# Performance work log

Measured on AMD Instinct MI355X. Metric: run time of the kernel, lower is better.

Reference implementation:

```python
import jax, jax.numpy as jnp
import numpy as np

PS = 14            # patch size
EMBED = 1024       # vision embed dim
LLM = 2048         # llm embed dim
DS = 2             # downsample factor
B = 8
GRID = 64          # H = W = 64 patches per image
MAX_POS = 4096
ROPE_THETA = 10000.0


def _rope_cache(dim, max_pos, base):
    inv_freq = 1.0 / (base ** (jnp.arange(0, dim, 2, dtype=jnp.float32) / dim))
    t = jnp.arange(max_pos, dtype=jnp.float32)
    freqs = jnp.outer(t, inv_freq)  # [max_pos, dim//2]
    return jnp.cos(freqs), jnp.sin(freqs)


def setup_inputs() -> dict:
    key = jax.random.key(0)
    ks = jax.random.split(key, 5)
    n_total = B * GRID * GRID
    pixel_values = jax.random.normal(ks[0], (n_total, 3, PS, PS), jnp.float32)
    patch_w = jax.random.normal(ks[1], (EMBED, 3, PS, PS), jnp.float32) * (1.0 / np.sqrt(3 * PS * PS))
    patch_b = jax.random.normal(ks[2], (EMBED,), jnp.float32) * 0.02
    dense_w = jax.random.normal(ks[3], (LLM, EMBED, DS, DS), jnp.float32) * (1.0 / np.sqrt(EMBED * DS * DS))
    dense_b = jax.random.normal(ks[4], (LLM,), jnp.float32) * 0.02
    rope_dim = EMBED // 2
    cos_x, sin_x = _rope_cache(rope_dim, MAX_POS, ROPE_THETA)
    cos_y, sin_y = _rope_cache(rope_dim, MAX_POS, ROPE_THETA)
    grid_hw = jnp.full((B, 2), GRID, dtype=jnp.int32)
    return {"pixel_values": pixel_values, "grid_hw": grid_hw,
            "patch_w": patch_w, "patch_b": patch_b,
            "dense_w": dense_w, "dense_b": dense_b,
            "cos_x": cos_x, "sin_x": sin_x, "cos_y": cos_y, "sin_y": sin_y}


def _apply_rotary_1d(x, cos_c, sin_c, pos):
    # x: [N, d], cos_c/sin_c: [max_pos, d//2], pos: [N] int
    c = cos_c[pos]  # gather: [N, d//2]
    s = sin_c[pos]
    x1 = x[:, 0::2]
    x2 = x[:, 1::2]
    o1 = x1 * c - x2 * s
    o2 = x1 * s + x2 * c
    return jnp.stack([o1, o2], axis=-1).reshape(x.shape)  # re-interleave


def _positions(grid_np):
    # grid metadata is static host-side data; build per-patch (x, y) coords
    xs, ys = [], []
    for h, w in grid_np:
        pid = np.arange(h * w)
        xs.append(pid % w)
        ys.append(pid // w)
    return jnp.asarray(np.concatenate(xs)), jnp.asarray(np.concatenate(ys))


def reference(pixel_values, grid_hw, patch_w, patch_b, dense_w, dense_b,
              cos_x, sin_x, cos_y, sin_y):
    grid_np = np.asarray(grid_hw)
    # patchify conv (kernel == stride == patch) is a per-patch linear proj
    pe = jnp.einsum('nchw,echw->ne', pixel_values, patch_w) + patch_b  # [N, E]
    pe = jax.nn.gelu(pe, approximate=False)
    abs_x, abs_y = _positions(grid_np)
    half = EMBED // 2
    p1 = _apply_rotary_1d(pe[:, :half], cos_x, sin_x, abs_x)
    p2 = _apply_rotary_1d(pe[:, half:], cos_y, sin_y, abs_y)
    pe = jnp.concatenate([p1, p2], axis=-1)  # [N, E]
    # per-image downsample conv (kernel == stride == DS): 2x2 block linear
    outs = []
    cur = 0
    for h, w in grid_np:
        x = pe[cur:cur + h * w].reshape(h // DS, DS, w // DS, DS, EMBED)
        o = jnp.einsum('hpwqe,oepq->hwo', x, dense_w) + dense_b
        outs.append(o.reshape(-1, LLM))
        cur += h * w
    return jnp.concatenate(outs, axis=0)
```

## Files before the change

### kernel.cpp

```cpp
#include <hip/hip_runtime.h>
#include <cstdint>


using f16x8 = __attribute__((ext_vector_type(8))) _Float16;
using f32x4 = __attribute__((ext_vector_type(4))) float;

__device__ __forceinline__ void gload_lds16(const void* g, void* l) {
  __builtin_amdgcn_global_load_lds(
      reinterpret_cast<const __attribute__((address_space(1))) unsigned int*>(
          reinterpret_cast<uintptr_t>(g)),
      reinterpret_cast<__attribute__((address_space(3))) unsigned int*>(
          reinterpret_cast<uintptr_t>(l)),
      16, 0, 0);
}

#define BAR   asm volatile("s_barrier" ::: "memory")
#define LGKM0 asm volatile("s_waitcnt lgkmcnt(0)" ::: "memory")
#define VM0   asm volatile("s_waitcnt vmcnt(0)" ::: "memory")

#define KP 640


__global__ void conv_b1_kernel(const float* __restrict__ w1,
                               _Float16* __restrict__ h) {
  int i = blockIdx.x * 256 + threadIdx.x;
  if (i >= 1024 * KP) return;
  int e = i / KP;
  int k = i - e * KP;
  float v = (k < 588) ? w1[(size_t)e * 588 + k] : 0.0f;
  h[i] = (_Float16)v;
}

__global__ void conv_b2_kernel(const float* __restrict__ w2,
                               _Float16* __restrict__ h) {
  int i = blockIdx.x * 256 + threadIdx.x;
  int o   = i >> 12;
  int rem = i & 4095;
  int pq  = rem >> 10;
  int e   = rem & 1023;
  h[i] = (_Float16)w2[(size_t)o * 4096 + e * 4 + pq];
}

__global__ void conv_pix_kernel(const float* __restrict__ pix,
                                _Float16* __restrict__ h) {
  int i = blockIdx.x * 256 + threadIdx.x;
  if (i >= 32768 * (KP / 8)) return;
  int n = i / (KP / 8);
  int g = i - n * (KP / 8);
  int k0 = g * 8;
  f16x8 v;
  if (k0 + 8 <= 588) {
    const float4 x0 = *(const float4*)(pix + (size_t)n * 588 + k0);
    const float4 x1 = *(const float4*)(pix + (size_t)n * 588 + k0 + 4);
    v[0] = (_Float16)x0.x; v[1] = (_Float16)x0.y;
    v[2] = (_Float16)x0.z; v[3] = (_Float16)x0.w;
    v[4] = (_Float16)x1.x; v[5] = (_Float16)x1.y;
    v[6] = (_Float16)x1.z; v[7] = (_Float16)x1.w;
  } else {
#pragma unroll
    for (int j = 0; j < 8; ++j) {
      int k = k0 + j;
      v[j] = (k < 588) ? (_Float16)pix[(size_t)n * 588 + k] : (_Float16)0.0f;
    }
  }
  *(f16x8*)(h + (size_t)n * KP + k0) = v;
}


#define MFMA16(I0, J0, AV, BV)                                                \
  _Pragma("unroll") for (int i_ = 0; i_ < 4; ++i_)                            \
  _Pragma("unroll") for (int j_ = 0; j_ < 2; ++j_)                            \
  _Pragma("unroll") for (int k_ = 0; k_ < 2; ++k_)                            \
      acc[(I0) + i_][(J0) + j_] = __builtin_amdgcn_mfma_f32_16x16x32_f16(     \
          AV[i_][k_], BV[j_][k_], acc[(I0) + i_][(J0) + j_], 0, 0, 0);

#define TILE_BODY(sb)                                                         \
  {                                                                           \
    f16x8 a0[4][2], a1[4][2], vb0[2][2], vb1[2][2];                           \
    _Pragma("unroll") for (int i = 0; i < 4; ++i) {                           \
      a0[i][0] = *(const f16x8*)(lbase + (sb) + aoff + i * 2048 + so0);       \
      a0[i][1] = *(const f16x8*)(lbase + (sb) + aoff + i * 2048 + so1);       \
    }                                                                         \
    _Pragma("unroll") for (int j = 0; j < 2; ++j) {                           \
      vb0[j][0] = *(const f16x8*)(lbase + (sb) + boff + j * 2048 + so0);      \
      vb0[j][1] = *(const f16x8*)(lbase + (sb) + boff + j * 2048 + so1);      \
    }                                                                         \
    MFMA16(0, 0, a0, vb0);                                                    \
    _Pragma("unroll") for (int j = 0; j < 2; ++j) {                           \
      vb1[j][0] = *(const f16x8*)(lbase + (sb) + boff + (2+j) * 2048 + so0);  \
      vb1[j][1] = *(const f16x8*)(lbase + (sb) + boff + (2+j) * 2048 + so1);  \
    }                                                                         \
    MFMA16(0, 2, a0, vb1);                                                    \
    _Pragma("unroll") for (int i = 0; i < 4; ++i) {                           \
      a1[i][0] = *(const f16x8*)(lbase + (sb) + aoff + (4+i) * 2048 + so0);   \
      a1[i][1] = *(const f16x8*)(lbase + (sb) + aoff + (4+i) * 2048 + so1);   \
    }                                                                         \
    MFMA16(4, 2, a1, vb1);                                                    \
    MFMA16(4, 0, a1, vb0);                                                    \
  }


__global__ __launch_bounds__(512, 2) void patch_gemm9(
    const _Float16* __restrict__ pixf,
    const _Float16* __restrict__ b1w,
    const float* __restrict__ bias1,
    const float* __restrict__ cosx, const float* __restrict__ sinx,
    const float* __restrict__ cosy, const float* __restrict__ siny,
    _Float16* __restrict__ peM)
{
  __shared__ _Float16 lds[2][2][256][64];

  const int tid  = threadIdx.x;
  const int lane = tid & 63;
  const int wave = tid >> 6;
  const int wm = wave >> 2, wn = wave & 3;
  const int bm = blockIdx.x, bn = blockIdx.y;
  const int l15 = lane & 15;
  const int g   = lane >> 4;
  const int s7  = l15 & 7;

  const char* lbase = (const char*)lds;
  char*       lw    = (char*)lds;
  const unsigned aoff = (unsigned)(wm * 16384 + l15 * 128);
  const unsigned boff = (unsigned)(32768 + wn * 8192 + l15 * 128);
  const unsigned so0  = (unsigned)(((0 + g) ^ s7) * 16);
  const unsigned so1  = (unsigned)(((4 + g) ^ s7) * 16);

  const int bm256 = bm * 256, bn256 = bn * 256;
  const int srow = (wave * 4) * 8 + (lane >> 3);
  const int sgc  = (lane & 7) ^ (srow & 7);

  auto STAGE = [&](int s) {
    char* slot = lw + ((size_t)(s & 1) << 16);
    const int c0 = s * 64;
#pragma unroll
    for (int u = 0; u < 4; ++u) {
      const int row  = srow + u * 8;
      const int gcol = (lane & 7) ^ (row & 7);
      gload_lds16(pixf + (size_t)(bm256 + row) * KP + c0 + gcol * 8,
                  slot + (wave * 4 + u) * 1024);
      gload_lds16(b1w + (size_t)(bn256 + row) * KP + c0 + gcol * 8,
                  slot + 32768 + (wave * 4 + u) * 1024);
    }
  };
  (void)sgc;

  f32x4 acc[8][4] = {};

  STAGE(0); VM0; BAR;
#pragma unroll 2
  for (int s = 0; s < 10; ++s) {
    if (s + 1 < 10) STAGE(s + 1);
    const unsigned sb = (unsigned)((s & 1) << 16);
    __builtin_amdgcn_s_setprio(1);
    TILE_BODY(sb);
    __builtin_amdgcn_s_setprio(0);
    LGKM0; VM0; BAR;
  }

  const int md = (lane >> 4) * 4;
#pragma unroll
  for (int mf = 0; mf < 8; ++mf) {
#pragma unroll
    for (int r = 0; r < 4; ++r) {
      const int m = bm256 + wm * 128 + mf * 16 + md + r;
      const int pid  = m & 4095;
      const int yy = pid >> 6, xx = pid & 63;
      const int t  = (m >> 12) * 1024 + (yy >> 1) * 32 + (xx >> 1);
      const int pq = (yy & 1) * 2 + (xx & 1);
      _Float16* dst = peM + (size_t)t * 4096 + pq * 1024;
#pragma unroll
      for (int nf = 0; nf < 4; ++nf) {
        const int e = bn256 + wn * 64 + nf * 16 + l15;
        float v = acc[mf][nf][r] + bias1[e];
        v = 0.5f * v * (1.0f + erff(v * 0.70710678118654752f));
        const float pv = __shfl_xor(v, 1, 64);
        const int h2  = (e >= 512) ? 1 : 0;
        const int idx = (h2 ? (e - 512) : e) >> 1;
        const int pos = h2 ? ((pid >> 6) & 63) : (pid & 63);
        const float cc = (h2 ? cosy : cosx)[pos * 256 + idx];
        const float ss = (h2 ? siny : sinx)[pos * 256 + idx];
        const float o = ((lane & 1) == 0) ? (v * cc - pv * ss)
                                          : (pv * ss + v * cc);
        dst[e] = (_Float16)o;
      }
    }
  }
}


__global__ __launch_bounds__(512, 2) void dense_gemm9(
    const _Float16* __restrict__ aM,
    const _Float16* __restrict__ bM,
    const float* __restrict__ bias2, float* __restrict__ out)
{
  __shared__ _Float16 lds[2][2][256][64];

  const int tid  = threadIdx.x;
  const int lane = tid & 63;
  const int wave = tid >> 6;
  const int wm = wave >> 2, wn = wave & 3;
  const int bm = blockIdx.x, bn = blockIdx.y;
  const int l15 = lane & 15;
  const int g   = lane >> 4;
  const int s7  = l15 & 7;

  const char* lbase = (const char*)lds;
  char*       lw    = (char*)lds;
  const unsigned aoff = (unsigned)(wm * 16384 + l15 * 128);
  const unsigned boff = (unsigned)(32768 + wn * 8192 + l15 * 128);
  const unsigned so0  = (unsigned)(((0 + g) ^ s7) * 16);
  const unsigned so1  = (unsigned)(((4 + g) ^ s7) * 16);

  const int bm256 = bm * 256, bn256 = bn * 256;
  const int srow = (wave * 4) * 8 + (lane >> 3);

  auto STAGE = [&](int s) {
    char* slot = lw + ((size_t)(s & 1) << 16);
    const int c0 = s * 64;
#pragma unroll
    for (int u = 0; u < 4; ++u) {
      const int row  = srow + u * 8;
      const int gcol = (lane & 7) ^ (row & 7);
      gload_lds16(aM + (size_t)(bm256 + row) * 4096 + c0 + gcol * 8,
                  slot + (wave * 4 + u) * 1024);
      gload_lds16(bM + (size_t)(bn256 + row) * 4096 + c0 + gcol * 8,
                  slot + 32768 + (wave * 4 + u) * 1024);
    }
  };

  f32x4 acc[8][4] = {};

  STAGE(0); VM0; BAR;
#pragma unroll 2
  for (int s = 0; s < 64; ++s) {
    if (s + 1 < 64) STAGE(s + 1);
    const unsigned sb = (unsigned)((s & 1) << 16);
    __builtin_amdgcn_s_setprio(1);
    TILE_BODY(sb);
    __builtin_amdgcn_s_setprio(0);
    LGKM0; VM0; BAR;
  }

  const int md = (lane >> 4) * 4;
  const int r0 = bm256 + wm * 128;
  const int c0 = bn256 + wn * 64;
#pragma unroll
  for (int nf = 0; nf < 4; ++nf) {
    const int o = c0 + nf * 16 + l15;
    const float bs = bias2[o];
#pragma unroll
    for (int mf = 0; mf < 8; ++mf) {
      const int t_ = r0 + mf * 16 + md;
#pragma unroll
      for (int r = 0; r < 4; ++r)
        out[(size_t)(t_ + r) * 2048 + o] = acc[mf][nf][r] + bs;
    }
  }
}


extern "C" void kernel_launch(void* const* d_in, const int* in_sizes, int n_in,
                              void* d_out, int out_size, void* d_ws, size_t ws_size,
                              hipStream_t stream) {
  const float* pix  = (const float*)d_in[0];
  const float* w1   = (const float*)d_in[2];
  const float* b1   = (const float*)d_in[3];
  const float* w2   = (const float*)d_in[4];
  const float* b2   = (const float*)d_in[5];
  const float* cosx = (const float*)d_in[6];
  const float* sinx = (const float*)d_in[7];
  const float* cosy = (const float*)d_in[8];
  const float* siny = (const float*)d_in[9];
  float* out = (float*)d_out;

  _Float16* ws = (_Float16*)d_ws;
  const size_t PE_N  = (size_t)8192 * 4096;
  const size_t B1_N  = (size_t)1024 * KP;
  const size_t B2_N  = (size_t)2048 * 4096;
  _Float16* peM  = ws;
  _Float16* b1h  = peM + PE_N;
  _Float16* b2h  = b1h + B1_N;
  _Float16* pixf = b2h + B2_N;

  conv_b1_kernel<<<dim3((1024 * KP + 255) / 256), dim3(256), 0, stream>>>(w1, b1h);
  conv_b2_kernel<<<dim3(32768), dim3(256), 0, stream>>>(w2, b2h);
  conv_pix_kernel<<<dim3((32768 * (KP / 8) + 255) / 256), dim3(256), 0, stream>>>(pix, pixf);
  patch_gemm9<<<dim3(128, 4), dim3(512), 0, stream>>>(
      pixf, b1h, b1, cosx, sinx, cosy, siny, peM);
  dense_gemm9<<<dim3(32, 8), dim3(512), 0, stream>>>(
      peM, b2h, b2, out);
}
```

Measured before the change: 290.8 us.

## Use 4-wave 128x128 warp tiles in dense GEMM and vectorize weight conversion

The dense GEMM drops from 8 waves with 128x64 per-wave tiles to 4 waves with 128x128 per-wave tiles (64 accumulators). Each wave now stages twice as many rows. The goal is more MFMA work per LDS fragment load and better register reuse. The cost is heavy register pressure at one block per CU, with fewer waves left to hide latency. The dense_w fp16 conversion now reads float4 and writes four strided outputs per thread, which cuts the number of blocks launched.

```diff
diff --git a/kernel.cpp b/kernel.cpp
--- a/kernel.cpp
+++ b/kernel.cpp
@@ -33,12 +33,14 @@
 
 __global__ void conv_b2_kernel(const float* __restrict__ w2,
                                _Float16* __restrict__ h) {
-  int i = blockIdx.x * 256 + threadIdx.x;
-  int o   = i >> 12;
-  int rem = i & 4095;
-  int pq  = rem >> 10;
-  int e   = rem & 1023;
-  h[i] = (_Float16)w2[(size_t)o * 4096 + e * 4 + pq];
+  int j = blockIdx.x * 256 + threadIdx.x;
+  int o = j >> 10;
+  int e = j & 1023;
+  const float4 v = *(const float4*)(w2 + (size_t)o * 4096 + e * 4);
+  h[(size_t)o * 4096 + 0 * 1024 + e] = (_Float16)v.x;
+  h[(size_t)o * 4096 + 1 * 1024 + e] = (_Float16)v.y;
+  h[(size_t)o * 4096 + 2 * 1024 + e] = (_Float16)v.z;
+  h[(size_t)o * 4096 + 3 * 1024 + e] = (_Float16)v.w;
 }
 
 __global__ void conv_pix_kernel(const float* __restrict__ pix,
@@ -99,7 +101,6 @@
     MFMA16(4, 0, a1, vb0);                                                    \
   }
 
-
 __global__ __launch_bounds__(512, 2) void patch_gemm9(
     const _Float16* __restrict__ pixf,
     const _Float16* __restrict__ b1w,
@@ -128,7 +129,6 @@
 
   const int bm256 = bm * 256, bn256 = bn * 256;
   const int srow = (wave * 4) * 8 + (lane >> 3);
-  const int sgc  = (lane & 7) ^ (srow & 7);
 
   auto STAGE = [&](int s) {
     char* slot = lw + ((size_t)(s & 1) << 16);
@@ -143,7 +143,6 @@
                   slot + 32768 + (wave * 4 + u) * 1024);
     }
   };
-  (void)sgc;
 
   f32x4 acc[8][4] = {};
 
@@ -177,7 +176,7 @@
         const float pv = __shfl_xor(v, 1, 64);
         const int h2  = (e >= 512) ? 1 : 0;
         const int idx = (h2 ? (e - 512) : e) >> 1;
-        const int pos = h2 ? ((pid >> 6) & 63) : (pid & 63);
+        const int pos = h2 ? yy : xx;
         const float cc = (h2 ? cosy : cosx)[pos * 256 + idx];
         const float ss = (h2 ? siny : sinx)[pos * 256 + idx];
         const float o = ((lane & 1) == 0) ? (v * cc - pv * ss)
@@ -189,7 +188,7 @@
 }
 
 
-__global__ __launch_bounds__(512, 2) void dense_gemm9(
+__global__ __launch_bounds__(256, 1) void dense_gemm10(
     const _Float16* __restrict__ aM,
     const _Float16* __restrict__ bM,
     const float* __restrict__ bias2, float* __restrict__ out)
@@ -199,7 +198,7 @@
   const int tid  = threadIdx.x;
   const int lane = tid & 63;
   const int wave = tid >> 6;
-  const int wm = wave >> 2, wn = wave & 3;
+  const int wm = wave >> 1, wn = wave & 1;
   const int bm = blockIdx.x, bn = blockIdx.y;
   const int l15 = lane & 15;
   const int g   = lane >> 4;
@@ -208,45 +207,59 @@
   const char* lbase = (const char*)lds;
   char*       lw    = (char*)lds;
   const unsigned aoff = (unsigned)(wm * 16384 + l15 * 128);
-  const unsigned boff = (unsigned)(32768 + wn * 8192 + l15 * 128);
+  const unsigned boff = (unsigned)(32768 + wn * 16384 + l15 * 128);
   const unsigned so0  = (unsigned)(((0 + g) ^ s7) * 16);
   const unsigned so1  = (unsigned)(((4 + g) ^ s7) * 16);
 
   const int bm256 = bm * 256, bn256 = bn * 256;
-  const int srow = (wave * 4) * 8 + (lane >> 3);
+  const int srow = wave * 64 + (lane >> 3);
 
   auto STAGE = [&](int s) {
     char* slot = lw + ((size_t)(s & 1) << 16);
     const int c0 = s * 64;
 #pragma unroll
-    for (int u = 0; u < 4; ++u) {
+    for (int u = 0; u < 8; ++u) {
       const int row  = srow + u * 8;
       const int gcol = (lane & 7) ^ (row & 7);
       gload_lds16(aM + (size_t)(bm256 + row) * 4096 + c0 + gcol * 8,
-                  slot + (wave * 4 + u) * 1024);
+                  slot + (wave * 8 + u) * 1024);
       gload_lds16(bM + (size_t)(bn256 + row) * 4096 + c0 + gcol * 8,
-                  slot + 32768 + (wave * 4 + u) * 1024);
+                  slot + 32768 + (wave * 8 + u) * 1024);
     }
   };
 
-  f32x4 acc[8][4] = {};
+  f32x4 acc[8][8] = {};
 
   STAGE(0); VM0; BAR;
 #pragma unroll 2
   for (int s = 0; s < 64; ++s) {
     if (s + 1 < 64) STAGE(s + 1);
     const unsigned sb = (unsigned)((s & 1) << 16);
-    __builtin_amdgcn_s_setprio(1);
-    TILE_BODY(sb);
-    __builtin_amdgcn_s_setprio(0);
+#pragma unroll
+    for (int ks = 0; ks < 2; ++ks) {
+      const unsigned so = ks ? so1 : so0;
+      f16x8 a[8], b[8];
+#pragma unroll
+      for (int i = 0; i < 8; ++i)
+        a[i] = *(const f16x8*)(lbase + sb + aoff + i * 2048 + so);
+#pragma unroll
+      for (int j = 0; j < 8; ++j)
+        b[j] = *(const f16x8*)(lbase + sb + boff + j * 2048 + so);
+#pragma unroll
+      for (int i = 0; i < 8; ++i)
+#pragma unroll
+        for (int j = 0; j < 8; ++j)
+          acc[i][j] = __builtin_amdgcn_mfma_f32_16x16x32_f16(
+              a[i], b[j], acc[i][j], 0, 0, 0);
+    }
     LGKM0; VM0; BAR;
   }
 
   const int md = (lane >> 4) * 4;
   const int r0 = bm256 + wm * 128;
-  const int c0 = bn256 + wn * 64;
-#pragma unroll
-  for (int nf = 0; nf < 4; ++nf) {
+  const int c0 = bn256 + wn * 128;
+#pragma unroll
+  for (int nf = 0; nf < 8; ++nf) {
     const int o = c0 + nf * 16 + l15;
     const float bs = bias2[o];
 #pragma unroll
@@ -284,10 +297,10 @@
   _Float16* pixf = b2h + B2_N;
 
   conv_b1_kernel<<<dim3((1024 * KP + 255) / 256), dim3(256), 0, stream>>>(w1, b1h);
-  conv_b2_kernel<<<dim3(32768), dim3(256), 0, stream>>>(w2, b2h);
+  conv_b2_kernel<<<dim3(8192), dim3(256), 0, stream>>>(w2, b2h);
   conv_pix_kernel<<<dim3((32768 * (KP / 8) + 255) / 256), dim3(256), 0, stream>>>(pix, pixf);
   patch_gemm9<<<dim3(128, 4), dim3(512), 0, stream>>>(
       pixf, b1h, b1, cosx, sinx, cosy, siny, peM);
-  dense_gemm9<<<dim3(32, 8), dim3(512), 0, stream>>>(
+  dense_gemm10<<<dim3(32, 8), dim3(256), 0, stream>>>(
       peM, b2h, b2, out);
 }
```

After: 457.7 us. +57.4%, slower.

## Fuse pixel fp32-to-fp16 conversion into patch GEMM and merge weight conversion kernels

Applied to the files above, without the earlier changes.

Removes the separate pixel conversion pass: the patch GEMM now loads fp32 pixels into registers, converts them to fp16 and writes them to swizzled LDS, and prefetches the next stage during the MFMA loop. This avoids writing and re-reading a padded fp16 copy of the pixels. The two weight conversion kernels are merged into one launch, and the w2 transpose now reads float4 vectors. In exchange the GEMM carries extra registers for the prefetch, and the A-tile path now uses ordinary loads plus LDS stores instead of direct global-to-LDS loads, with a wait inside the loop.

```diff
diff --git a/kernel.cpp b/kernel.cpp
--- a/kernel.cpp
+++ b/kernel.cpp
@@ -3,6 +3,7 @@
 
 
 using f16x8 = __attribute__((ext_vector_type(8))) _Float16;
+using f16x4 = __attribute__((ext_vector_type(4))) _Float16;
 using f32x4 = __attribute__((ext_vector_type(4))) float;
 
 __device__ __forceinline__ void gload_lds16(const void* g, void* l) {
@@ -21,49 +22,27 @@
 #define KP 640
 
 
-__global__ void conv_b1_kernel(const float* __restrict__ w1,
-                               _Float16* __restrict__ h) {
-  int i = blockIdx.x * 256 + threadIdx.x;
-  if (i >= 1024 * KP) return;
-  int e = i / KP;
-  int k = i - e * KP;
-  float v = (k < 588) ? w1[(size_t)e * 588 + k] : 0.0f;
-  h[i] = (_Float16)v;
-}
-
-__global__ void conv_b2_kernel(const float* __restrict__ w2,
-                               _Float16* __restrict__ h) {
-  int i = blockIdx.x * 256 + threadIdx.x;
-  int o   = i >> 12;
-  int rem = i & 4095;
-  int pq  = rem >> 10;
-  int e   = rem & 1023;
-  h[i] = (_Float16)w2[(size_t)o * 4096 + e * 4 + pq];
-}
-
-__global__ void conv_pix_kernel(const float* __restrict__ pix,
-                                _Float16* __restrict__ h) {
-  int i = blockIdx.x * 256 + threadIdx.x;
-  if (i >= 32768 * (KP / 8)) return;
-  int n = i / (KP / 8);
-  int g = i - n * (KP / 8);
-  int k0 = g * 8;
-  f16x8 v;
-  if (k0 + 8 <= 588) {
-    const float4 x0 = *(const float4*)(pix + (size_t)n * 588 + k0);
-    const float4 x1 = *(const float4*)(pix + (size_t)n * 588 + k0 + 4);
-    v[0] = (_Float16)x0.x; v[1] = (_Float16)x0.y;
-    v[2] = (_Float16)x0.z; v[3] = (_Float16)x0.w;
-    v[4] = (_Float16)x1.x; v[5] = (_Float16)x1.y;
-    v[6] = (_Float16)x1.z; v[7] = (_Float16)x1.w;
+__global__ void conv_w_kernel(const float* __restrict__ w1,
+                              const float* __restrict__ w2,
+                              _Float16* __restrict__ h1,
+                              _Float16* __restrict__ h2) {
+  const int bid = blockIdx.x;
+  if (bid < 2560) {
+    int i = bid * 256 + threadIdx.x;
+    int e = i / KP;
+    int k = i - e * KP;
+    float v = (k < 588) ? w1[(size_t)e * 588 + k] : 0.0f;
+    h1[i] = (_Float16)v;
   } else {
-#pragma unroll
-    for (int j = 0; j < 8; ++j) {
-      int k = k0 + j;
-      v[j] = (k < 588) ? (_Float16)pix[(size_t)n * 588 + k] : (_Float16)0.0f;
-    }
-  }
-  *(f16x8*)(h + (size_t)n * KP + k0) = v;
+    int j = (bid - 2560) * 256 + threadIdx.x;
+    int o = j >> 10;
+    int e = j & 1023;
+    const float4 v = *(const float4*)(w2 + (size_t)o * 4096 + e * 4);
+    h2[(size_t)o * 4096 + e]        = (_Float16)v.x;
+    h2[(size_t)o * 4096 + 1024 + e] = (_Float16)v.y;
+    h2[(size_t)o * 4096 + 2048 + e] = (_Float16)v.z;
+    h2[(size_t)o * 4096 + 3072 + e] = (_Float16)v.w;
+  }
 }
 
 
@@ -100,8 +79,8 @@
   }
 
 
-__global__ __launch_bounds__(512, 2) void patch_gemm9(
-    const _Float16* __restrict__ pixf,
+__global__ __launch_bounds__(512, 2) void patch_gemm11(
+    const float* __restrict__ pix,
     const _Float16* __restrict__ b1w,
     const float* __restrict__ bias1,
     const float* __restrict__ cosx, const float* __restrict__ sinx,
@@ -127,35 +106,86 @@
   const unsigned so1  = (unsigned)(((4 + g) ^ s7) * 16);
 
   const int bm256 = bm * 256, bn256 = bn * 256;
-  const int srow = (wave * 4) * 8 + (lane >> 3);
-  const int sgc  = (lane & 7) ^ (srow & 7);
-
-  auto STAGE = [&](int s) {
-    char* slot = lw + ((size_t)(s & 1) << 16);
+  const int srow = wave * 32 + (lane >> 3);
+  const int acol = lane & 15;
+  const int arw  = wave * 32 + (lane >> 4);
+
+  auto LOADA = [&](int s, float4 (&ar)[8]) {
+    const bool full = (s < 9);
+#pragma unroll
+    for (int u = 0; u < 8; ++u) {
+      const int row = arw + u * 4;
+      const float* p = pix + (size_t)(bm256 + row) * 588 + s * 64 + acol * 4;
+      if (full || acol < 3) ar[u] = *(const float4*)p;
+      else ar[u] = make_float4(0.f, 0.f, 0.f, 0.f);
+    }
+  };
+  auto WRITEA = [&](int s, float4 (&ar)[8]) {
+    char* slot = lw + ((size_t)((s) & 1) << 16);
+    const int c   = acol >> 1;
+    const int sub = acol & 1;
+#pragma unroll
+    for (int u = 0; u < 8; ++u) {
+      const int row = arw + u * 4;
+      f16x4 v;
+      v[0] = (_Float16)ar[u].x; v[1] = (_Float16)ar[u].y;
+      v[2] = (_Float16)ar[u].z; v[3] = (_Float16)ar[u].w;
+      *(f16x4*)(slot + row * 128 + ((c ^ (row & 7)) * 16 + sub * 8)) = v;
+    }
+  };
+  auto STAGE_B = [&](int s) {
+    char* slot = lw + ((size_t)((s) & 1) << 16);
     const int c0 = s * 64;
 #pragma unroll
     for (int u = 0; u < 4; ++u) {
       const int row  = srow + u * 8;
       const int gcol = (lane & 7) ^ (row & 7);
-      gload_lds16(pixf + (size_t)(bm256 + row) * KP + c0 + gcol * 8,
-                  slot + (wave * 4 + u) * 1024);
       gload_lds16(b1w + (size_t)(bn256 + row) * KP + c0 + gcol * 8,
                   slot + 32768 + (wave * 4 + u) * 1024);
     }
   };
-  (void)sgc;
 
   f32x4 acc[8][4] = {};
-
-  STAGE(0); VM0; BAR;
-#pragma unroll 2
+  float4 areg[8];
+
+  LOADA(0, areg); STAGE_B(0);
+  VM0; WRITEA(0, areg); LGKM0; BAR;
+
   for (int s = 0; s < 10; ++s) {
-    if (s + 1 < 10) STAGE(s + 1);
     const unsigned sb = (unsigned)((s & 1) << 16);
+    const bool st = (s + 1 < 10);
+    if (st) { LOADA(s + 1, areg); STAGE_B(s + 1); }
+    f16x8 a0[4][2], a1[4][2], vb0[2][2], vb1[2][2];
     __builtin_amdgcn_s_setprio(1);
-    TILE_BODY(sb);
+#pragma unroll
+    for (int i = 0; i < 4; ++i) {
+      a0[i][0] = *(const f16x8*)(lbase + sb + aoff + i * 2048 + so0);
+      a0[i][1] = *(const f16x8*)(lbase + sb + aoff + i * 2048 + so1);
+    }
+#pragma unroll
+    for (int j = 0; j < 2; ++j) {
+      vb0[j][0] = *(const f16x8*)(lbase + sb + boff + j * 2048 + so0);
+      vb0[j][1] = *(const f16x8*)(lbase + sb + boff + j * 2048 + so1);
+    }
+    MFMA16(0, 0, a0, vb0);
+#pragma unroll
+    for (int j = 0; j < 2; ++j) {
+      vb1[j][0] = *(const f16x8*)(lbase + sb + boff + (2 + j) * 2048 + so0);
+      vb1[j][1] = *(const f16x8*)(lbase + sb + boff + (2 + j) * 2048 + so1);
+    }
+    MFMA16(0, 2, a0, vb1);
+#pragma unroll
+    for (int i = 0; i < 4; ++i) {
+      a1[i][0] = *(const f16x8*)(lbase + sb + aoff + (4 + i) * 2048 + so0);
+      a1[i][1] = *(const f16x8*)(lbase + sb + aoff + (4 + i) * 2048 + so1);
+    }
     __builtin_amdgcn_s_setprio(0);
-    LGKM0; VM0; BAR;
+    if (st) { VM0; WRITEA(s + 1, areg); }
+    __builtin_amdgcn_s_setprio(1);
+    MFMA16(4, 2, a1, vb1);
+    MFMA16(4, 0, a1, vb0);
+    __builtin_amdgcn_s_setprio(0);
+    LGKM0; BAR;
   }
 
   const int md = (lane >> 4) * 4;
@@ -177,7 +207,7 @@
         const float pv = __shfl_xor(v, 1, 64);
         const int h2  = (e >= 512) ? 1 : 0;
         const int idx = (h2 ? (e - 512) : e) >> 1;
-        const int pos = h2 ? ((pid >> 6) & 63) : (pid & 63);
+        const int pos = h2 ? yy : xx;
         const float cc = (h2 ? cosy : cosx)[pos * 256 + idx];
         const float ss = (h2 ? siny : sinx)[pos * 256 + idx];
         const float o = ((lane & 1) == 0) ? (v * cc - pv * ss)
@@ -277,17 +307,13 @@
   _Float16* ws = (_Float16*)d_ws;
   const size_t PE_N  = (size_t)8192 * 4096;
   const size_t B1_N  = (size_t)1024 * KP;
-  const size_t B2_N  = (size_t)2048 * 4096;
   _Float16* peM  = ws;
   _Float16* b1h  = peM + PE_N;
   _Float16* b2h  = b1h + B1_N;
-  _Float16* pixf = b2h + B2_N;
-
-  conv_b1_kernel<<<dim3((1024 * KP + 255) / 256), dim3(256), 0, stream>>>(w1, b1h);
-  conv_b2_kernel<<<dim3(32768), dim3(256), 0, stream>>>(w2, b2h);
-  conv_pix_kernel<<<dim3((32768 * (KP / 8) + 255) / 256), dim3(256), 0, stream>>>(pix, pixf);
-  patch_gemm9<<<dim3(128, 4), dim3(512), 0, stream>>>(
-      pixf, b1h, b1, cosx, sinx, cosy, siny, peM);
+
+  conv_w_kernel<<<dim3(2560 + 8192), dim3(256), 0, stream>>>(w1, w2, b1h, b2h);
+  patch_gemm11<<<dim3(128, 4), dim3(512), 0, stream>>>(
+      pix, b1h, b1, cosx, sinx, cosy, siny, peM);
   dense_gemm9<<<dim3(32, 8), dim3(512), 0, stream>>>(
       peM, b2h, b2, out);
 }
```

Measured after the change: 262.9 us. 9.6% less time.

## Fuse conversion kernels and single-buffer patch GEMM LDS

Applied to the files above, without the earlier changes.

Merges the three fp32-to-fp16 conversion kernels into one launch, and vectorizes the dense-weight transpose with a float4 read per thread. The patch GEMM drops from a double-buffered to a single-buffered LDS layout (64KB instead of 128KB), which may allow more resident blocks per CU, but the next K-stage is no longer prefetched and each step now waits on its global loads. The rope position lookup reuses the already computed coordinates.

```diff
diff --git a/kernel.cpp b/kernel.cpp
--- a/kernel.cpp
+++ b/kernel.cpp
@@ -21,49 +21,50 @@
 #define KP 640
 
 
-__global__ void conv_b1_kernel(const float* __restrict__ w1,
-                               _Float16* __restrict__ h) {
-  int i = blockIdx.x * 256 + threadIdx.x;
-  if (i >= 1024 * KP) return;
-  int e = i / KP;
-  int k = i - e * KP;
-  float v = (k < 588) ? w1[(size_t)e * 588 + k] : 0.0f;
-  h[i] = (_Float16)v;
-}
-
-__global__ void conv_b2_kernel(const float* __restrict__ w2,
-                               _Float16* __restrict__ h) {
-  int i = blockIdx.x * 256 + threadIdx.x;
-  int o   = i >> 12;
-  int rem = i & 4095;
-  int pq  = rem >> 10;
-  int e   = rem & 1023;
-  h[i] = (_Float16)w2[(size_t)o * 4096 + e * 4 + pq];
-}
-
-__global__ void conv_pix_kernel(const float* __restrict__ pix,
-                                _Float16* __restrict__ h) {
-  int i = blockIdx.x * 256 + threadIdx.x;
-  if (i >= 32768 * (KP / 8)) return;
-  int n = i / (KP / 8);
-  int g = i - n * (KP / 8);
-  int k0 = g * 8;
-  f16x8 v;
-  if (k0 + 8 <= 588) {
-    const float4 x0 = *(const float4*)(pix + (size_t)n * 588 + k0);
-    const float4 x1 = *(const float4*)(pix + (size_t)n * 588 + k0 + 4);
-    v[0] = (_Float16)x0.x; v[1] = (_Float16)x0.y;
-    v[2] = (_Float16)x0.z; v[3] = (_Float16)x0.w;
-    v[4] = (_Float16)x1.x; v[5] = (_Float16)x1.y;
-    v[6] = (_Float16)x1.z; v[7] = (_Float16)x1.w;
+__global__ void conv_w_kernel(const float* __restrict__ w1,
+                              const float* __restrict__ w2,
+                              const float* __restrict__ pix,
+                              _Float16* __restrict__ h1,
+                              _Float16* __restrict__ h2,
+                              _Float16* __restrict__ pf) {
+  const int bid = blockIdx.x;
+  if (bid < 2560) {
+    int i = bid * 256 + threadIdx.x;
+    int e = i / KP;
+    int k = i - e * KP;
+    float v = (k < 588) ? w1[(size_t)e * 588 + k] : 0.0f;
+    h1[i] = (_Float16)v;
+  } else if (bid < 2560 + 8192) {
+    int j = (bid - 2560) * 256 + threadIdx.x;
+    int o = j >> 10;
+    int e = j & 1023;
+    const float4 v = *(const float4*)(w2 + (size_t)o * 4096 + e * 4);
+    h2[(size_t)o * 4096 + e]        = (_Float16)v.x;
+    h2[(size_t)o * 4096 + 1024 + e] = (_Float16)v.y;
+    h2[(size_t)o * 4096 + 2048 + e] = (_Float16)v.z;
+    h2[(size_t)o * 4096 + 3072 + e] = (_Float16)v.w;
   } else {
-#pragma unroll
-    for (int j = 0; j < 8; ++j) {
-      int k = k0 + j;
-      v[j] = (k < 588) ? (_Float16)pix[(size_t)n * 588 + k] : (_Float16)0.0f;
-    }
-  }
-  *(f16x8*)(h + (size_t)n * KP + k0) = v;
+    int j = (bid - 2560 - 8192) * 256 + threadIdx.x;
+    int n = j / (KP / 8);
+    int g = j - n * (KP / 8);
+    int k0 = g * 8;
+    f16x8 v;
+    if (k0 + 8 <= 588) {
+      const float4 x0 = *(const float4*)(pix + (size_t)n * 588 + k0);
+      const float4 x1 = *(const float4*)(pix + (size_t)n * 588 + k0 + 4);
+      v[0] = (_Float16)x0.x; v[1] = (_Float16)x0.y;
+      v[2] = (_Float16)x0.z; v[3] = (_Float16)x0.w;
+      v[4] = (_Float16)x1.x; v[5] = (_Float16)x1.y;
+      v[6] = (_Float16)x1.z; v[7] = (_Float16)x1.w;
+    } else {
+#pragma unroll
+      for (int t = 0; t < 8; ++t) {
+        int k = k0 + t;
+        v[t] = (k < 588) ? (_Float16)pix[(size_t)n * 588 + k] : (_Float16)0.0f;
+      }
+    }
+    *(f16x8*)(pf + (size_t)n * KP + k0) = v;
+  }
 }
 
 
@@ -100,7 +101,7 @@
   }
 
 
-__global__ __launch_bounds__(512, 2) void patch_gemm9(
+__global__ __launch_bounds__(512, 2) void patch_gemm13(
     const _Float16* __restrict__ pixf,
     const _Float16* __restrict__ b1w,
     const float* __restrict__ bias1,
@@ -108,7 +109,7 @@
     const float* __restrict__ cosy, const float* __restrict__ siny,
     _Float16* __restrict__ peM)
 {
-  __shared__ _Float16 lds[2][2][256][64];
+  __shared__ _Float16 lds[2][256][64];
 
   const int tid  = threadIdx.x;
   const int lane = tid & 63;
@@ -127,35 +128,30 @@
   const unsigned so1  = (unsigned)(((4 + g) ^ s7) * 16);
 
   const int bm256 = bm * 256, bn256 = bn * 256;
-  const int srow = (wave * 4) * 8 + (lane >> 3);
-  const int sgc  = (lane & 7) ^ (srow & 7);
+  const int srow = wave * 32 + (lane >> 3);
 
   auto STAGE = [&](int s) {
-    char* slot = lw + ((size_t)(s & 1) << 16);
     const int c0 = s * 64;
 #pragma unroll
     for (int u = 0; u < 4; ++u) {
       const int row  = srow + u * 8;
       const int gcol = (lane & 7) ^ (row & 7);
       gload_lds16(pixf + (size_t)(bm256 + row) * KP + c0 + gcol * 8,
-                  slot + (wave * 4 + u) * 1024);
+                  lw + (wave * 4 + u) * 1024);
       gload_lds16(b1w + (size_t)(bn256 + row) * KP + c0 + gcol * 8,
-                  slot + 32768 + (wave * 4 + u) * 1024);
+                  lw + 32768 + (wave * 4 + u) * 1024);
     }
   };
-  (void)sgc;
 
   f32x4 acc[8][4] = {};
 
-  STAGE(0); VM0; BAR;
-#pragma unroll 2
   for (int s = 0; s < 10; ++s) {
-    if (s + 1 < 10) STAGE(s + 1);
-    const unsigned sb = (unsigned)((s & 1) << 16);
+    STAGE(s);
+    VM0; BAR;
     __builtin_amdgcn_s_setprio(1);
-    TILE_BODY(sb);
+    TILE_BODY(0u);
     __builtin_amdgcn_s_setprio(0);
-    LGKM0; VM0; BAR;
+    LGKM0; BAR;
   }
 
   const int md = (lane >> 4) * 4;
@@ -177,7 +173,7 @@
         const float pv = __shfl_xor(v, 1, 64);
         const int h2  = (e >= 512) ? 1 : 0;
         const int idx = (h2 ? (e - 512) : e) >> 1;
-        const int pos = h2 ? ((pid >> 6) & 63) : (pid & 63);
+        const int pos = h2 ? yy : xx;
         const float cc = (h2 ? cosy : cosx)[pos * 256 + idx];
         const float ss = (h2 ? siny : sinx)[pos * 256 + idx];
         const float o = ((lane & 1) == 0) ? (v * cc - pv * ss)
@@ -283,10 +279,10 @@
   _Float16* b2h  = b1h + B1_N;
   _Float16* pixf = b2h + B2_N;
 
-  conv_b1_kernel<<<dim3((1024 * KP + 255) / 256), dim3(256), 0, stream>>>(w1, b1h);
-  conv_b2_kernel<<<dim3(32768), dim3(256), 0, stream>>>(w2, b2h);
-  conv_pix_kernel<<<dim3((32768 * (KP / 8) + 255) / 256), dim3(256), 0, stream>>>(pix, pixf);
-  patch_gemm9<<<dim3(128, 4), dim3(512), 0, stream>>>(
+  const int pix_blocks = (32768 * (KP / 8)) / 256;
+  conv_w_kernel<<<dim3(2560 + 8192 + pix_blocks), dim3(256), 0, stream>>>(
+      w1, w2, pix, b1h, b2h, pixf);
+  patch_gemm13<<<dim3(128, 4), dim3(512), 0, stream>>>(
       pixf, b1h, b1, cosx, sinx, cosy, siny, peM);
   dense_gemm9<<<dim3(32, 8), dim3(512), 0, stream>>>(
       peM, b2h, b2, out);
```

Result: faster. 270.7 us (-6.9%).
